# Performance work log

Hardware: AMD Instinct MI355X
Metric: run time of the kernel (lower is better)

## Reference

```python
import jax, jax.numpy as jnp
import numpy as np

B, S, D, L = 4, 2048, 1024, 4  # batch, seq_len, d_model, num_layers


def setup_inputs() -> dict:
    key = jax.random.key(0)
    ks = jax.random.split(key, 6)
    w = lambda k, shape: jax.random.normal(k, shape, jnp.float32) * 0.02
    return {
        "x": jax.random.normal(ks[0], (B, S, D), jnp.float32),
        # stacked per-layer parameters [L, ...]
        "Wkqv": w(ks[1], (L, D, 3 * D)),
        "Wm1": w(ks[2], (L, D, 2 * D)), "bm1": jnp.zeros((L, 2 * D), jnp.float32),
        "Wm2": w(ks[3], (L, D, D)), "bm2": jnp.zeros((L, D), jnp.float32),
        "gn_g": jnp.ones((L, D), jnp.float32), "gn_b": jnp.zeros((L, D), jnp.float32),
        "Wf1": w(ks[4], (L, D, 2 * D)), "bf1": jnp.zeros((L, 2 * D), jnp.float32),
        "Wf2": w(ks[5], (L, 2 * D, D)), "bf2": jnp.zeros((L, D), jnp.float32),
        "ln_g": jnp.ones((L, D), jnp.float32), "ln_b": jnp.zeros((L, D), jnp.float32),
    }


def _retention(x, wkqv):
    d = x.shape[-1]
    k, q, v = jnp.split(x @ wkqv, 3, axis=-1)            # each [B,S,D]
    qkt = jnp.einsum('bid,bjd->bij', q, k) / jnp.sqrt(jnp.float32(d))
    s = x.shape[1]
    row_norm = 1.0 + jnp.sqrt(jnp.arange(s, dtype=x.dtype))[None, :, None]
    r = jnp.tril(qkt) / row_norm                          # causal, per-row sqrt-index norm
    denom = jnp.clip(jnp.abs(r.sum(-1, keepdims=True)), 1.0, None)
    r = r / denom
    return jnp.einsum('bij,bjd->bid', r, v)


def _groupnorm1(y, g, b, eps=1e-5):
    # torch GroupNorm(1, D) on [B, D, S]: normalize over (D, S) per batch element
    mu = y.mean(axis=(1, 2), keepdims=True)
    var = y.var(axis=(1, 2), keepdims=True)
    return (y - mu) / jnp.sqrt(var + eps) * g + b


def _layernorm(y, g, b, eps=1e-5):
    mu = y.mean(-1, keepdims=True)
    var = y.var(-1, keepdims=True)
    return (y - mu) / jnp.sqrt(var + eps) * g + b


def reference(x, Wkqv, Wm1, bm1, Wm2, bm2, gn_g, gn_b, Wf1, bf1, Wf2, bf2, ln_g, ln_b):
    def block(h, p):
        wk, w1, b1, w2, b2, gg, gb, wf1, bf1_, wf2, bf2_, lg, lb = p
        r = _retention(h, wk)
        m = r @ w1 + b1
        a, gate = jnp.split(m, 2, axis=-1)                # SwiGLU
        m = (a * jax.nn.silu(gate)) @ w2 + b2
        m = _groupnorm1(m, gg, gb)
        y = m + h
        f = jax.nn.gelu(y @ wf1 + bf1_, approximate=False) @ wf2 + bf2_
        return _layernorm(f + y, lg, lb), None

    params = (Wkqv, Wm1, bm1, Wm2, bm2, gn_g, gn_b, Wf1, bf1, Wf2, bf2, ln_g, ln_b)
    out, _ = jax.lax.scan(block, x, params)
    return out
```

## Files before the change

kernel.cpp:

```cpp
#include <hip/hip_runtime.h>


constexpr int Bb = 4, Ss = 2048, Dd = 1024, Ll = 4;
constexpr int BSm = Bb * Ss;

typedef short bf16x8 __attribute__((ext_vector_type(8)));
typedef float f32x4  __attribute__((ext_vector_type(4)));
typedef unsigned short us;

__device__ __forceinline__ us bf16_rn(float x) {
    unsigned int u = __float_as_uint(x);
    u += 0x7FFFu + ((u >> 16) & 1u);
    return (us)(u >> 16);
}
__device__ __forceinline__ float bf2f(us h) {
    return __uint_as_float(((unsigned int)h) << 16);
}
__device__ __forceinline__ void fsplit(float v, us& h, us& l) {
    h = bf16_rn(v);
    l = bf16_rn(v - bf2f(h));
}

#define GLL(g, l) __builtin_amdgcn_global_load_lds( \
    (const __attribute__((address_space(1))) void*)(g), \
    (__attribute__((address_space(3))) void*)(l), 16, 0, 0)

#define MFMA16(a, b, c) __builtin_amdgcn_mfma_f32_16x16x32_bf16(a, b, c, 0, 0, 0)

template<int OUT, bool HAS_BIAS, int ACT, bool CAUSAL, bool CK, bool ROWSCALE>
__global__ __launch_bounds__(256, 2) void gemm3(
    const us* __restrict__ Ahg, const us* __restrict__ Alg, int lda, long sA,
    const us* __restrict__ Bhg, const us* __restrict__ Blg, int ldb, long sB,
    const float* __restrict__ bias,
    float* __restrict__ Cf, us* __restrict__ Ch, us* __restrict__ Cl,
    int ldc, long sC,
    const float* __restrict__ drec, int K)
{
    __shared__ __align__(16) char lds[2 * 32768];

    if (CAUSAL && blockIdx.x > blockIdx.y) return;
    const int t = threadIdx.x, z = blockIdx.z;
    const int row0 = blockIdx.y * 128, col0 = blockIdx.x * 128;
    Ahg += (size_t)z * sA;  Alg += (size_t)z * sA;
    Bhg += (size_t)z * sB;  Blg += (size_t)z * sB;

    const int srow = t >> 2;
    const int scg  = ((t & 3) ^ ((t >> 3) & 3)) * 8;
    const us* pAh = Ahg + (size_t)(row0 + srow) * lda + scg;
    const us* pAl = Alg + (size_t)(row0 + srow) * lda + scg;
    const us* pBh = Bhg + (size_t)(col0 + srow) * ldb + scg;
    const us* pBl = Blg + (size_t)(col0 + srow) * ldb + scg;
    const size_t a64 = (size_t)64 * lda, b64 = (size_t)64 * ldb;
    const int wb = (t >> 6) * 1024;

    auto stage = [&](int kt) {
        const int k0 = kt * 32;
        char* base = lds + (kt & 1) * 32768 + wb;
        GLL(pAh + k0,       base + 0 * 8192);
        GLL(pAh + k0 + a64, base + 0 * 8192 + 4096);
        GLL(pAl + k0,       base + 1 * 8192);
        GLL(pAl + k0 + a64, base + 1 * 8192 + 4096);
        GLL(pBh + k0,       base + 2 * 8192);
        GLL(pBh + k0 + b64, base + 2 * 8192 + 4096);
        GLL(pBl + k0,       base + 3 * 8192);
        GLL(pBl + k0 + b64, base + 3 * 8192 + 4096);
    };

    const int ln = t & 63, lr = ln & 15, q = ln >> 4;
    const int w  = t >> 6, wm = w >> 1, wn = w & 1;
    const int xq = (q ^ ((lr >> 1) & 3)) * 16;
    int offA[4], offB[4];
    #pragma unroll
    for (int m = 0; m < 4; ++m) offA[m] = (wm * 64 + m * 16 + lr) * 64 + xq;
    #pragma unroll
    for (int n = 0; n < 4; ++n) offB[n] = (wn * 64 + n * 16 + lr) * 64 + xq;

    f32x4 acc[4][4] = {};

    int Keff = K;
    if (CK) { int ke = row0 + 128; Keff = ke < K ? ke : K; }
    const int NT = Keff >> 5;

    stage(0);
    for (int kt = 0; kt < NT; ++kt) {
        __syncthreads();
        if (kt + 1 < NT) stage(kt + 1);
        const char* base = lds + (kt & 1) * 32768;
        bf16x8 ah[4], al8[4], bh[4], bl8[4];
        #pragma unroll
        for (int m = 0; m < 4; ++m) {
            ah[m]  = *reinterpret_cast<const bf16x8*>(base + 0 * 8192 + offA[m]);
            al8[m] = *reinterpret_cast<const bf16x8*>(base + 1 * 8192 + offA[m]);
        }
        #pragma unroll
        for (int n = 0; n < 4; ++n) {
            bh[n]  = *reinterpret_cast<const bf16x8*>(base + 2 * 8192 + offB[n]);
            bl8[n] = *reinterpret_cast<const bf16x8*>(base + 3 * 8192 + offB[n]);
        }
        #pragma unroll
        for (int n = 0; n < 4; ++n) {
            #pragma unroll
            for (int m = 0; m < 4; ++m) acc[m][n] = MFMA16(ah[m],  bh[n],  acc[m][n]);
            #pragma unroll
            for (int m = 0; m < 4; ++m) acc[m][n] = MFMA16(ah[m],  bl8[n], acc[m][n]);
            #pragma unroll
            for (int m = 0; m < 4; ++m) acc[m][n] = MFMA16(al8[m], bh[n],  acc[m][n]);
        }
    }

    const float* dz = drec + (size_t)z * Ss;
    #pragma unroll
    for (int n = 0; n < 4; ++n) {
        const int col = col0 + wn * 64 + n * 16 + lr;
        const float bv = HAS_BIAS ? bias[col] : 0.0f;
        #pragma unroll
        for (int m = 0; m < 4; ++m) {
            #pragma unroll
            for (int j = 0; j < 4; ++j) {
                const int row = row0 + wm * 64 + m * 16 + 4 * q + j;
                float v = acc[m][n][j] + bv;
                if (ACT == 1)
                    v = 0.5f * v * (1.0f + erff(v * 0.70710678118f));
                if (CAUSAL)
                    v = (col <= row)
                        ? v * (1.0f / (32.0f * (1.0f + sqrtf((float)row))))
                        : 0.0f;
                if (ROWSCALE) v *= dz[row];
                const size_t idx = (size_t)z * sC + (size_t)row * ldc + col;
                if (OUT == 0) {
                    Cf[idx] = v;
                } else {
                    us h_, l_;
                    fsplit(v, h_, l_);
                    Ch[idx] = h_;
                    Cl[idx] = l_;
                }
            }
        }
    }
}

template<int OUT, bool HAS_BIAS, int ACT>
__global__ __launch_bounds__(512, 2) void gemm3w(
    const us* __restrict__ Ahg, const us* __restrict__ Alg, int lda,
    const us* __restrict__ Bhg, const us* __restrict__ Blg, int ldb,
    const float* __restrict__ bias,
    float* __restrict__ Cf, us* __restrict__ Ch, us* __restrict__ Cl,
    int ldc, int K)
{
    __shared__ __align__(16) char lds[2 * 65536];

    const int t = threadIdx.x;
    const int row0 = blockIdx.y * 256, col0 = blockIdx.x * 256;

    const int srow = t >> 2;
    const int scg  = ((t & 3) ^ ((t >> 3) & 3)) * 8;
    const us* pAh = Ahg + (size_t)(row0 + srow) * lda + scg;
    const us* pAl = Alg + (size_t)(row0 + srow) * lda + scg;
    const us* pBh = Bhg + (size_t)(col0 + srow) * ldb + scg;
    const us* pBl = Blg + (size_t)(col0 + srow) * ldb + scg;
    const size_t a128 = (size_t)128 * lda, b128 = (size_t)128 * ldb;
    const int wb = (t >> 6) * 1024;

    auto stage = [&](int kt) {
        const int k0 = kt * 32;
        char* base = lds + (kt & 1) * 65536 + wb;
        GLL(pAh + k0,        base + 0 * 16384);
        GLL(pAh + k0 + a128, base + 0 * 16384 + 8192);
        GLL(pAl + k0,        base + 1 * 16384);
        GLL(pAl + k0 + a128, base + 1 * 16384 + 8192);
        GLL(pBh + k0,        base + 2 * 16384);
        GLL(pBh + k0 + b128, base + 2 * 16384 + 8192);
        GLL(pBl + k0,        base + 3 * 16384);
        GLL(pBl + k0 + b128, base + 3 * 16384 + 8192);
    };

    const int ln = t & 63, lr = ln & 15, q = ln >> 4;
    const int w  = t >> 6, wm = w >> 2, wn = w & 3;
    const int xq = (q ^ ((lr >> 1) & 3)) * 16;
    int offA[8], offB[4];
    #pragma unroll
    for (int m = 0; m < 8; ++m)
        offA[m] = (m * 16 + lr) * 64 + xq + wm * 8192;
    #pragma unroll
    for (int n = 0; n < 4; ++n) {
        const int R = wn * 64 + n * 16 + lr;
        offB[n] = (R & 127) * 64 + xq + (R >> 7) * 8192;
    }

    f32x4 acc[8][4] = {};
    const int NT = K >> 5;

    stage(0);
    for (int kt = 0; kt < NT; ++kt) {
        __syncthreads();
        if (kt + 1 < NT) stage(kt + 1);
        const char* base = lds + (kt & 1) * 65536;
        bf16x8 ah[8], al8[8];
        #pragma unroll
        for (int m = 0; m < 8; ++m) {
            ah[m]  = *reinterpret_cast<const bf16x8*>(base + 0 * 16384 + offA[m]);
            al8[m] = *reinterpret_cast<const bf16x8*>(base + 1 * 16384 + offA[m]);
        }
        #pragma unroll
        for (int n = 0; n < 4; ++n) {
            bf16x8 bh  = *reinterpret_cast<const bf16x8*>(base + 2 * 16384 + offB[n]);
            bf16x8 bl8 = *reinterpret_cast<const bf16x8*>(base + 3 * 16384 + offB[n]);
            #pragma unroll
            for (int m = 0; m < 8; ++m) acc[m][n] = MFMA16(ah[m],  bh,  acc[m][n]);
            #pragma unroll
            for (int m = 0; m < 8; ++m) acc[m][n] = MFMA16(ah[m],  bl8, acc[m][n]);
            #pragma unroll
            for (int m = 0; m < 8; ++m) acc[m][n] = MFMA16(al8[m], bh,  acc[m][n]);
        }
    }

    #pragma unroll
    for (int n = 0; n < 4; ++n) {
        const int col = col0 + wn * 64 + n * 16 + lr;
        const float bv = HAS_BIAS ? bias[col] : 0.0f;
        #pragma unroll
        for (int m = 0; m < 8; ++m) {
            #pragma unroll
            for (int j = 0; j < 4; ++j) {
                const int row = row0 + wm * 128 + m * 16 + 4 * q + j;
                float v = acc[m][n][j] + bv;
                if (ACT == 1)
                    v = 0.5f * v * (1.0f + erff(v * 0.70710678118f));
                const size_t idx = (size_t)row * ldc + col;
                if (OUT == 0) {
                    Cf[idx] = v;
                } else {
                    us h_, l_;
                    fsplit(v, h_, l_);
                    Ch[idx] = h_;
                    Cl[idx] = l_;
                }
            }
        }
    }
}

__global__ __launch_bounds__(256) void split_k(
    const float* __restrict__ in, us* __restrict__ oh, us* __restrict__ ol)
{
    const size_t e = (size_t)blockIdx.x * 256 + threadIdx.x;
    float4 v = *reinterpret_cast<const float4*>(in + e * 4);
    ushort4 h4, l4;
    fsplit(v.x, h4.x, l4.x); fsplit(v.y, h4.y, l4.y);
    fsplit(v.z, h4.z, l4.z); fsplit(v.w, h4.w, l4.w);
    *reinterpret_cast<ushort4*>(oh + e * 4) = h4;
    *reinterpret_cast<ushort4*>(ol + e * 4) = l4;
}

__global__ __launch_bounds__(256) void tsplit_k(
    const float* __restrict__ in, long sin_,
    us* __restrict__ oh, us* __restrict__ ol, long sout, int H, int W)
{
    __shared__ float tile[32][33];
    const int z = blockIdx.z;
    in += (size_t)z * sin_;  oh += (size_t)z * sout;  ol += (size_t)z * sout;
    const int c0 = blockIdx.x * 32, r0 = blockIdx.y * 32;
    const int tr = threadIdx.x >> 3, tc = (threadIdx.x & 7) * 4;
    float4 v = *reinterpret_cast<const float4*>(in + (size_t)(r0 + tr) * W + c0 + tc);
    tile[tr][tc + 0] = v.x; tile[tr][tc + 1] = v.y;
    tile[tr][tc + 2] = v.z; tile[tr][tc + 3] = v.w;
    __syncthreads();
    ushort4 h4, l4;
    fsplit(tile[tc + 0][tr], h4.x, l4.x);
    fsplit(tile[tc + 1][tr], h4.y, l4.y);
    fsplit(tile[tc + 2][tr], h4.z, l4.z);
    fsplit(tile[tc + 3][tr], h4.w, l4.w);
    const size_t o = (size_t)(c0 + tr) * H + r0 + tc;
    *reinterpret_cast<ushort4*>(oh + o) = h4;
    *reinterpret_cast<ushort4*>(ol + o) = l4;
}

__global__ __launch_bounds__(256) void denom_k(
    const us* __restrict__ sph, const us* __restrict__ spl,
    float* __restrict__ drec)
{
    const int r = blockIdx.x, b = blockIdx.y, t = threadIdx.x;
    const us* ph = sph + ((size_t)b * Ss + r) * Ss;
    const us* pl = spl + ((size_t)b * Ss + r) * Ss;
    const int jmax = ((r >> 7) + 1) << 7;
    float s = 0.f;
    for (int j4 = t; j4 * 4 < jmax; j4 += 256) {
        ushort4 h = *reinterpret_cast<const ushort4*>(ph + j4 * 4);
        ushort4 lo = *reinterpret_cast<const ushort4*>(pl + j4 * 4);
        s += (bf2f(h.x) + bf2f(lo.x)) + (bf2f(h.y) + bf2f(lo.y))
           + (bf2f(h.z) + bf2f(lo.z)) + (bf2f(h.w) + bf2f(lo.w));
    }
    __shared__ float rs[256];
    rs[t] = s;
    __syncthreads();
    for (int off = 128; off > 0; off >>= 1) {
        if (t < off) rs[t] += rs[t + off];
        __syncthreads();
    }
    if (t == 0) drec[(size_t)b * Ss + r] = 1.0f / fmaxf(1.0f, fabsf(rs[0]));
}

__global__ __launch_bounds__(256) void swiglu_k(
    const float* __restrict__ m1, us* __restrict__ oh, us* __restrict__ ol)
{
    const size_t e = (size_t)blockIdx.x * 256 + threadIdx.x;
    const size_t row = e / (Dd / 4);
    const int c4 = (int)(e % (Dd / 4));
    const float* base = m1 + row * (2 * Dd);
    float4 a = *reinterpret_cast<const float4*>(base + c4 * 4);
    float4 g = *reinterpret_cast<const float4*>(base + Dd + c4 * 4);
    float o0 = a.x * (g.x / (1.f + expf(-g.x)));
    float o1 = a.y * (g.y / (1.f + expf(-g.y)));
    float o2 = a.z * (g.z / (1.f + expf(-g.z)));
    float o3 = a.w * (g.w / (1.f + expf(-g.w)));
    ushort4 h4, l4;
    fsplit(o0, h4.x, l4.x); fsplit(o1, h4.y, l4.y);
    fsplit(o2, h4.z, l4.z); fsplit(o3, h4.w, l4.w);
    const size_t o = row * Dd + c4 * 4;
    *reinterpret_cast<ushort4*>(oh + o) = h4;
    *reinterpret_cast<ushort4*>(ol + o) = l4;
}

__global__ __launch_bounds__(256) void gn_part_k(
    const float* __restrict__ m2, float* __restrict__ part)
{
    const int b = blockIdx.y, blk = blockIdx.x;
    const float* p = m2 + (size_t)b * Ss * Dd + (size_t)blk * 8192;
    float s = 0.f, ss = 0.f;
    for (int t = threadIdx.x; t < 2048; t += 256) {
        float4 v = *reinterpret_cast<const float4*>(p + (size_t)t * 4);
        s  += (v.x + v.y) + (v.z + v.w);
        ss += v.x * v.x + v.y * v.y + v.z * v.z + v.w * v.w;
    }
    __shared__ float rs[256], rss[256];
    rs[threadIdx.x] = s; rss[threadIdx.x] = ss;
    __syncthreads();
    for (int off = 128; off > 0; off >>= 1) {
        if (threadIdx.x < off) {
            rs[threadIdx.x]  += rs[threadIdx.x + off];
            rss[threadIdx.x] += rss[threadIdx.x + off];
        }
        __syncthreads();
    }
    if (threadIdx.x == 0) {
        part[(b * 256 + blk) * 2]     = rs[0];
        part[(b * 256 + blk) * 2 + 1] = rss[0];
    }
}

__global__ __launch_bounds__(256) void gn_final_k(
    const float* __restrict__ part, float* __restrict__ stats)
{
    const int b = blockIdx.x, t = threadIdx.x;
    float s  = part[(b * 256 + t) * 2];
    float ss = part[(b * 256 + t) * 2 + 1];
    __shared__ float rs[256], rss[256];
    rs[t] = s; rss[t] = ss;
    __syncthreads();
    for (int off = 128; off > 0; off >>= 1) {
        if (t < off) { rs[t] += rs[t + off]; rss[t] += rss[t + off]; }
        __syncthreads();
    }
    if (t == 0) {
        const float inv_n = 1.0f / (float)((size_t)Ss * Dd);
        float mean = rs[0] * inv_n;
        float var  = fmaxf(rss[0] * inv_n - mean * mean, 0.0f);
        stats[b * 2]     = mean;
        stats[b * 2 + 1] = rsqrtf(var + 1e-5f);
    }
}

__global__ __launch_bounds__(256) void gn_apply_k(
    const float* __restrict__ m2, const float* __restrict__ h,
    const float* __restrict__ g, const float* __restrict__ bta,
    const float* __restrict__ stats, float* __restrict__ y,
    us* __restrict__ yh, us* __restrict__ yl)
{
    const size_t e = (size_t)blockIdx.x * 256 + threadIdx.x;
    const int b  = (int)(e / ((size_t)Ss * Dd / 4));
    const int c4 = (int)(e % (Dd / 4));
    const float mean = stats[b * 2], istd = stats[b * 2 + 1];
    float4 m  = *reinterpret_cast<const float4*>(m2 + e * 4);
    float4 hh = *reinterpret_cast<const float4*>(h + e * 4);
    float4 g4 = *reinterpret_cast<const float4*>(g + c4 * 4);
    float4 b4 = *reinterpret_cast<const float4*>(bta + c4 * 4);
    float4 o;
    o.x = (m.x - mean) * istd * g4.x + b4.x + hh.x;
    o.y = (m.y - mean) * istd * g4.y + b4.y + hh.y;
    o.z = (m.z - mean) * istd * g4.z + b4.z + hh.z;
    o.w = (m.w - mean) * istd * g4.w + b4.w + hh.w;
    *reinterpret_cast<float4*>(y + e * 4) = o;
    ushort4 h4, l4;
    fsplit(o.x, h4.x, l4.x); fsplit(o.y, h4.y, l4.y);
    fsplit(o.z, h4.z, l4.z); fsplit(o.w, h4.w, l4.w);
    *reinterpret_cast<ushort4*>(yh + e * 4) = h4;
    *reinterpret_cast<ushort4*>(yl + e * 4) = l4;
}

template<bool SPLIT>
__global__ __launch_bounds__(256) void ln_k(
    const float* __restrict__ f2, const float* __restrict__ y,
    const float* __restrict__ g, const float* __restrict__ bta,
    float* __restrict__ out, us* __restrict__ oh, us* __restrict__ ol)
{
    const int row = blockIdx.x;
    const int t = threadIdx.x;
    float4 fv = *reinterpret_cast<const float4*>(f2 + (size_t)row * Dd + t * 4);
    float4 yv = *reinterpret_cast<const float4*>(y  + (size_t)row * Dd + t * 4);
    const float v0 = fv.x + yv.x, v1 = fv.y + yv.y;
    const float v2 = fv.z + yv.z, v3 = fv.w + yv.w;
    float s  = (v0 + v1) + (v2 + v3);
    float ss = v0 * v0 + v1 * v1 + v2 * v2 + v3 * v3;
    __shared__ float rs[256], rss[256];
    rs[t] = s; rss[t] = ss;
    __syncthreads();
    for (int off = 128; off > 0; off >>= 1) {
        if (t < off) { rs[t] += rs[t + off]; rss[t] += rss[t + off]; }
        __syncthreads();
    }
    const float mean = rs[0] * (1.0f / Dd);
    const float var  = fmaxf(rss[0] * (1.0f / Dd) - mean * mean, 0.0f);
    const float istd = rsqrtf(var + 1e-5f);
    float4 g4 = *reinterpret_cast<const float4*>(g + t * 4);
    float4 b4 = *reinterpret_cast<const float4*>(bta + t * 4);
    float4 o;
    o.x = (v0 - mean) * istd * g4.x + b4.x;
    o.y = (v1 - mean) * istd * g4.y + b4.y;
    o.z = (v2 - mean) * istd * g4.z + b4.z;
    o.w = (v3 - mean) * istd * g4.w + b4.w;
    *reinterpret_cast<float4*>(out + (size_t)row * Dd + t * 4) = o;
    if (SPLIT) {
        ushort4 h4, l4;
        fsplit(o.x, h4.x, l4.x); fsplit(o.y, h4.y, l4.y);
        fsplit(o.z, h4.z, l4.z); fsplit(o.w, h4.w, l4.w);
        const size_t e = (size_t)row * Dd + t * 4;
        *reinterpret_cast<ushort4*>(oh + e) = h4;
        *reinterpret_cast<ushort4*>(ol + e) = l4;
    }
}

extern "C" void kernel_launch(void* const* d_in, const int* in_sizes, int n_in,
                              void* d_out, int out_size, void* d_ws, size_t ws_size,
                              hipStream_t stream)
{
    const float* x    = (const float*)d_in[0];
    const float* Wkqv = (const float*)d_in[1];
    const float* Wm1  = (const float*)d_in[2];
    const float* bm1  = (const float*)d_in[3];
    const float* Wm2  = (const float*)d_in[4];
    const float* bm2  = (const float*)d_in[5];
    const float* gng  = (const float*)d_in[6];
    const float* gnb  = (const float*)d_in[7];
    const float* Wf1  = (const float*)d_in[8];
    const float* bf1  = (const float*)d_in[9];
    const float* Wf2  = (const float*)d_in[10];
    const float* bf2  = (const float*)d_in[11];
    const float* lng  = (const float*)d_in[12];
    const float* lnb  = (const float*)d_in[13];

    char* wsb = (char*)d_ws;
    const size_t MiB = 1024 * 1024;
    auto SL = [&](int i) { return wsb + (size_t)i * 16 * MiB; };

    float* hbuf   = (float*)SL(0);
    us* h_hi      = (us*)SL(2);
    us* h_lo      = (us*)SL(3);
    us* qk_hi     = (us*)SL(4);
    us* qk_lo     = (us*)SL(6);
    float* vbuf   = (float*)SL(8);
    us* WtA_hi    = (us*)SL(10);
    us* WtA_lo    = (us*)(SL(10) + 6 * MiB);
    us* vT_hi     = (us*)SL(2);
    us* vT_lo     = (us*)SL(3);
    us* sp_hi     = (us*)SL(8);
    us* sp_lo     = (us*)SL(10);
    float* drec   = (float*)SL(4);
    us* ret_hi    = (us*)SL(6);
    us* ret_lo    = (us*)SL(7);
    us* Wt1_hi    = (us*)SL(2);
    us* Wt1_lo    = (us*)(SL(2) + 4 * MiB);
    float* m1     = (float*)SL(8);
    us* sw_hi     = (us*)SL(4);
    us* sw_lo     = (us*)SL(5);
    us* Wt2_hi    = (us*)SL(2);
    us* Wt2_lo    = (us*)(SL(2) + 2 * MiB);
    float* m2     = (float*)SL(10);
    float* part   = (float*)SL(2);
    float* stats  = (float*)(SL(2) + 1 * MiB);
    float* ybuf   = (float*)SL(8);
    us* y_hi      = (us*)SL(4);
    us* y_lo      = (us*)SL(5);
    us* Wtf1_hi   = (us*)SL(6);
    us* Wtf1_lo   = (us*)(SL(6) + 4 * MiB);
    us* f1_hi     = (us*)SL(10);
    us* f1_lo     = (us*)SL(2);
    us* Wtf2_hi   = (us*)SL(6);
    us* Wtf2_lo   = (us*)(SL(6) + 4 * MiB);
    float* f2     = (float*)SL(4);

    for (int l = 0; l < Ll; ++l) {
        const float* h = (l == 0) ? x : hbuf;
        if (l == 0)
            split_k<<<8192, 256, 0, stream>>>(x, h_hi, h_lo);

        tsplit_k<<<dim3(3 * Dd / 32, Dd / 32, 1), 256, 0, stream>>>(
            Wkqv + (size_t)l * Dd * 3 * Dd, 0, WtA_hi, WtA_lo, 0, Dd, 3 * Dd);
        gemm3w<1, false, 0><<<dim3(8, 32), 512, 0, stream>>>(
            h_hi, h_lo, Dd, WtA_hi, WtA_lo, Dd, nullptr,
            nullptr, qk_hi, qk_lo, 2 * Dd, Dd);
        gemm3<0, false, 0, false, false, false><<<dim3(8, 64, 1), 256, 0, stream>>>(
            h_hi, h_lo, Dd, 0,
            WtA_hi + (size_t)2 * Dd * Dd, WtA_lo + (size_t)2 * Dd * Dd, Dd, 0,
            nullptr, vbuf, nullptr, nullptr, Dd, 0, drec, Dd);
        tsplit_k<<<dim3(Dd / 32, Ss / 32, Bb), 256, 0, stream>>>(
            vbuf, (long)Ss * Dd, vT_hi, vT_lo, (long)Dd * Ss, Ss, Dd);

        gemm3<1, false, 0, true, false, false><<<dim3(16, 16, Bb), 256, 0, stream>>>(
            qk_hi + Dd, qk_lo + Dd, 2 * Dd, (long)Ss * 2 * Dd,
            qk_hi,      qk_lo,      2 * Dd, (long)Ss * 2 * Dd,
            nullptr, nullptr, sp_hi, sp_lo, Ss, (long)Ss * Ss, drec, Dd);
        denom_k<<<dim3(Ss, Bb), 256, 0, stream>>>(sp_hi, sp_lo, drec);
        gemm3<1, false, 0, false, true, true><<<dim3(8, 16, Bb), 256, 0, stream>>>(
            sp_hi, sp_lo, Ss, (long)Ss * Ss,
            vT_hi, vT_lo, Ss, (long)Dd * Ss,
            nullptr, nullptr, ret_hi, ret_lo, Dd, (long)Ss * Dd, drec, Ss);

        tsplit_k<<<dim3(2 * Dd / 32, Dd / 32, 1), 256, 0, stream>>>(
            Wm1 + (size_t)l * Dd * 2 * Dd, 0, Wt1_hi, Wt1_lo, 0, Dd, 2 * Dd);
        gemm3w<0, true, 0><<<dim3(8, 32), 512, 0, stream>>>(
            ret_hi, ret_lo, Dd, Wt1_hi, Wt1_lo, Dd,
            bm1 + (size_t)l * 2 * Dd, m1, nullptr, nullptr, 2 * Dd, Dd);
        swiglu_k<<<8192, 256, 0, stream>>>(m1, sw_hi, sw_lo);
        tsplit_k<<<dim3(Dd / 32, Dd / 32, 1), 256, 0, stream>>>(
            Wm2 + (size_t)l * Dd * Dd, 0, Wt2_hi, Wt2_lo, 0, Dd, Dd);
        gemm3<0, true, 0, false, false, false><<<dim3(8, 64, 1), 256, 0, stream>>>(
            sw_hi, sw_lo, Dd, 0, Wt2_hi, Wt2_lo, Dd, 0,
            bm2 + (size_t)l * Dd, m2, nullptr, nullptr, Dd, 0, drec, Dd);

        gn_part_k<<<dim3(256, Bb), 256, 0, stream>>>(m2, part);
        gn_final_k<<<Bb, 256, 0, stream>>>(part, stats);
        gn_apply_k<<<8192, 256, 0, stream>>>(
            m2, h, gng + (size_t)l * Dd, gnb + (size_t)l * Dd, stats,
            ybuf, y_hi, y_lo);

        tsplit_k<<<dim3(2 * Dd / 32, Dd / 32, 1), 256, 0, stream>>>(
            Wf1 + (size_t)l * Dd * 2 * Dd, 0, Wtf1_hi, Wtf1_lo, 0, Dd, 2 * Dd);
        gemm3w<1, true, 1><<<dim3(8, 32), 512, 0, stream>>>(
            y_hi, y_lo, Dd, Wtf1_hi, Wtf1_lo, Dd,
            bf1 + (size_t)l * 2 * Dd,
            nullptr, f1_hi, f1_lo, 2 * Dd, Dd);
        tsplit_k<<<dim3(Dd / 32, 2 * Dd / 32, 1), 256, 0, stream>>>(
            Wf2 + (size_t)l * 2 * Dd * Dd, 0, Wtf2_hi, Wtf2_lo, 0, 2 * Dd, Dd);
        gemm3<0, true, 0, false, false, false><<<dim3(8, 64, 1), 256, 0, stream>>>(
            f1_hi, f1_lo, 2 * Dd, 0, Wtf2_hi, Wtf2_lo, 2 * Dd, 0,
            bf2 + (size_t)l * Dd, f2, nullptr, nullptr, Dd, 0, drec, 2 * Dd);

        if (l == Ll - 1)
            ln_k<false><<<BSm, 256, 0, stream>>>(
                f2, ybuf, lng + (size_t)l * Dd, lnb + (size_t)l * Dd,
                (float*)d_out, nullptr, nullptr);
        else
            ln_k<true><<<BSm, 256, 0, stream>>>(
                f2, ybuf, lng + (size_t)l * Dd, lnb + (size_t)l * Dd,
                hbuf, h_hi, h_lo);
    }
}
```

Before: 3.318 ms.

## Prefetch two K-tiles ahead with explicit waitcnt and split barriers in GEMM loops

Both bf16-split GEMM kernels now issue loads for two tiles up front and, once the current tile's LDS fragments are read into registers, start the global-to-LDS copy for tile kt+2. The single __syncthreads is replaced by a partial vmcnt wait plus s_barrier before the reads and an lgkmcnt(0) wait plus barrier after them. MFMA sections run at raised wave priority via s_setprio. The goal is to keep more memory traffic in flight and overlap it with MFMA work, at the cost of more registers in the second kernel and a vmcnt(8) threshold that is only correct if stage() issues exactly that many loads.

```diff
diff --git a/kernel.cpp b/kernel.cpp
--- a/kernel.cpp
+++ b/kernel.cpp
@@ -82,9 +82,13 @@
     const int NT = Keff >> 5;
 
     stage(0);
+    stage(1);
     for (int kt = 0; kt < NT; ++kt) {
-        __syncthreads();
-        if (kt + 1 < NT) stage(kt + 1);
+        if (kt < NT - 1) asm volatile("s_waitcnt vmcnt(8)" ::: "memory");
+        else             asm volatile("s_waitcnt vmcnt(0)" ::: "memory");
+        __builtin_amdgcn_sched_barrier(0);
+        __builtin_amdgcn_s_barrier();
+        __builtin_amdgcn_sched_barrier(0);
         const char* base = lds + (kt & 1) * 32768;
         bf16x8 ah[4], al8[4], bh[4], bl8[4];
         #pragma unroll
@@ -97,6 +101,11 @@
             bh[n]  = *reinterpret_cast<const bf16x8*>(base + 2 * 8192 + offB[n]);
             bl8[n] = *reinterpret_cast<const bf16x8*>(base + 3 * 8192 + offB[n]);
         }
+        asm volatile("s_waitcnt lgkmcnt(0)" ::: "memory");
+        __builtin_amdgcn_sched_barrier(0);
+        __builtin_amdgcn_s_barrier();
+        if (kt + 2 < NT) stage(kt + 2);
+        __builtin_amdgcn_s_setprio(1);
         #pragma unroll
         for (int n = 0; n < 4; ++n) {
             #pragma unroll
@@ -106,6 +115,7 @@
             #pragma unroll
             for (int m = 0; m < 4; ++m) acc[m][n] = MFMA16(al8[m], bh[n],  acc[m][n]);
         }
+        __builtin_amdgcn_s_setprio(0);
     }
 
     const float* dz = drec + (size_t)z * Ss;
@@ -192,11 +202,15 @@
     const int NT = K >> 5;
 
     stage(0);
+    stage(1);
     for (int kt = 0; kt < NT; ++kt) {
-        __syncthreads();
-        if (kt + 1 < NT) stage(kt + 1);
+        if (kt < NT - 1) asm volatile("s_waitcnt vmcnt(8)" ::: "memory");
+        else             asm volatile("s_waitcnt vmcnt(0)" ::: "memory");
+        __builtin_amdgcn_sched_barrier(0);
+        __builtin_amdgcn_s_barrier();
+        __builtin_amdgcn_sched_barrier(0);
         const char* base = lds + (kt & 1) * 65536;
-        bf16x8 ah[8], al8[8];
+        bf16x8 ah[8], al8[8], bh[4], bl8[4];
         #pragma unroll
         for (int m = 0; m < 8; ++m) {
             ah[m]  = *reinterpret_cast<const bf16x8*>(base + 0 * 16384 + offA[m]);
@@ -204,15 +218,24 @@
         }
         #pragma unroll
         for (int n = 0; n < 4; ++n) {
-            bf16x8 bh  = *reinterpret_cast<const bf16x8*>(base + 2 * 16384 + offB[n]);
-            bf16x8 bl8 = *reinterpret_cast<const bf16x8*>(base + 3 * 16384 + offB[n]);
-            #pragma unroll
-            for (int m = 0; m < 8; ++m) acc[m][n] = MFMA16(ah[m],  bh,  acc[m][n]);
-            #pragma unroll
-            for (int m = 0; m < 8; ++m) acc[m][n] = MFMA16(ah[m],  bl8, acc[m][n]);
-            #pragma unroll
-            for (int m = 0; m < 8; ++m) acc[m][n] = MFMA16(al8[m], bh,  acc[m][n]);
-        }
+            bh[n]  = *reinterpret_cast<const bf16x8*>(base + 2 * 16384 + offB[n]);
+            bl8[n] = *reinterpret_cast<const bf16x8*>(base + 3 * 16384 + offB[n]);
+        }
+        asm volatile("s_waitcnt lgkmcnt(0)" ::: "memory");
+        __builtin_amdgcn_sched_barrier(0);
+        __builtin_amdgcn_s_barrier();
+        if (kt + 2 < NT) stage(kt + 2);
+        __builtin_amdgcn_s_setprio(1);
+        #pragma unroll
+        for (int n = 0; n < 4; ++n) {
+            #pragma unroll
+            for (int m = 0; m < 8; ++m) acc[m][n] = MFMA16(ah[m],  bh[n],  acc[m][n]);
+            #pragma unroll
+            for (int m = 0; m < 8; ++m) acc[m][n] = MFMA16(ah[m],  bl8[n], acc[m][n]);
+            #pragma unroll
+            for (int m = 0; m < 8; ++m) acc[m][n] = MFMA16(al8[m], bh[n],  acc[m][n]);
+        }
+        __builtin_amdgcn_s_setprio(0);
     }
 
     #pragma unroll
```

Result: slower. 3.436 ms (+3.6%).
